# Performance work log

Hardware: AMD Instinct MI355X
Metric: run time of the kernel (lower is better)

The kernel has to match this reference:

```python
import jax, jax.numpy as jnp
import numpy as np

B, O, D = 64, 36, 512
G1, G2 = 512, 512  # interactor sizes
F1, F2 = 512, 512  # aggregator sizes
BN_EPS = 1e-5


def setup_inputs() -> dict:
    key = jax.random.key(0)
    ks = jax.random.split(key, 10)
    sc = 0.02
    return {
        "objs": jax.random.normal(ks[0], (B, O, D), jnp.float32),
        "W1": jax.random.normal(ks[1], (G1, 2 * D), jnp.float32) * sc,
        "b1": jax.random.normal(ks[2], (G1,), jnp.float32) * sc,
        "W2": jax.random.normal(ks[3], (G2, G1), jnp.float32) * sc,
        "b2": jax.random.normal(ks[4], (G2,), jnp.float32) * sc,
        "gamma": jnp.ones((G2,), jnp.float32),
        "beta": jnp.zeros((G2,), jnp.float32),
        "W3": jax.random.normal(ks[5], (F1, G2), jnp.float32) * sc,
        "b3": jax.random.normal(ks[6], (F1,), jnp.float32) * sc,
        "W4": jax.random.normal(ks[7], (F2, F1), jnp.float32) * sc,
        "b4": jax.random.normal(ks[8], (F2,), jnp.float32) * sc,
    }


def reference(objs, W1, b1, W2, b2, gamma, beta, W3, b3, W4, b4):
    b, o, d = objs.shape
    # make_pairs: x_full[b,k,m] = concat(v[b,m], v[b,k]) -> (b, o*o, 2d)
    v_i = jnp.broadcast_to(objs[:, None, :, :], (b, o, o, d))  # varies over m
    v_j = jnp.broadcast_to(objs[:, :, None, :], (b, o, o, d))  # varies over k
    pairs = jnp.concatenate([v_i, v_j], axis=-1).reshape(b, o * o, 2 * d)
    # interaction MLP g
    h = jax.nn.relu(jnp.einsum('bpc,gc->bpg', pairs, W1) + b1)
    x_pairs = jax.nn.relu(jnp.einsum('bpg,hg->bph', h, W2) + b2)
    # sum over pairs, BatchNorm1d (training mode: batch stats, biased var)
    s = x_pairs.sum(axis=1)  # (b, G2)
    mean = s.mean(axis=0)
    var = ((s - mean) ** 2).mean(axis=0)
    sn = (s - mean) / jnp.sqrt(var + BN_EPS) * gamma + beta
    # aggregation MLP f
    a = jax.nn.relu(sn @ W3.T + b3)
    agg = jax.nn.relu(a @ W4.T + b4)
    return agg, x_pairs
```

## Files before the change

### kernel.cpp

```cpp
#include <hip/hip_runtime.h>
#include <cstdint>
#include <cstddef>

#define B_  64
#define O_  36
#define D_  512
#define P_  (O_*O_)
#define BO_ (B_*O_)

typedef short s8v __attribute__((ext_vector_type(8)));
typedef float f4v __attribute__((ext_vector_type(4)));

__device__ __forceinline__ void bsplit(float x, short& hi, short& lo) {
    unsigned u = __float_as_uint(x);
    unsigned r = (u + 0x7FFFu + ((u >> 16) & 1u)) >> 16;
    hi = (short)r;
    float hf = __uint_as_float(r << 16);
    float d = x - hf;
    unsigned u2 = __float_as_uint(d);
    unsigned r2 = (u2 + 0x7FFFu + ((u2 >> 16) & 1u)) >> 16;
    lo = (short)r2;
}

__global__ __launch_bounds__(256) void w2split(
    const float* __restrict__ W2, short* __restrict__ hi, short* __restrict__ lo)
{
    const int i = (blockIdx.x * 256 + threadIdx.x) * 4;
    const float4 w = *(const float4*)&W2[i];
    short h0, l0, h1, l1, h2, l2, h3, l3;
    bsplit(w.x, h0, l0); bsplit(w.y, h1, l1);
    bsplit(w.z, h2, l2); bsplit(w.w, h3, l3);
    *(short4*)&hi[i] = make_short4(h0, h1, h2, h3);
    *(short4*)&lo[i] = make_short4(l0, l1, l2, l3);
}

__global__ __launch_bounds__(256) void w1split(
    const float* __restrict__ W1, short* __restrict__ hi, short* __restrict__ lo)
{
    const int i = (blockIdx.x * 256 + threadIdx.x) * 4;
    const int n = i >> 9, d = i & 511;
    const float4 w = *(const float4*)&W1[(size_t)(n & 511) * 1024 + ((n >> 9) << 9) + d];
    short h0, l0, h1, l1, h2, l2, h3, l3;
    bsplit(w.x, h0, l0); bsplit(w.y, h1, l1);
    bsplit(w.z, h2, l2); bsplit(w.w, h3, l3);
    *(short4*)&hi[i] = make_short4(h0, h1, h2, h3);
    *(short4*)&lo[i] = make_short4(l0, l1, l2, l3);
}

__global__ __launch_bounds__(256, 2) void uv_mfma(
    const float* __restrict__ objs,
    const short* __restrict__ W1h, const short* __restrict__ W1l,
    float* __restrict__ U, float* __restrict__ V)
{
    __shared__ short Ah[128 * 40];
    __shared__ short Al[128 * 40];
    __shared__ short Bh[128 * 40];
    __shared__ short Bl[128 * 40];

    const int tid  = threadIdx.x;
    const int lane = tid & 63;
    const int wid  = tid >> 6;
    const int wr   = wid >> 1, wc = wid & 1;
    const int rowbase = blockIdx.y * 128;
    const int colbase = blockIdx.x * 128;

    const int srow = tid >> 1;
    const int skq  = (tid & 1) * 8;
    const float* Xrow  = objs + (size_t)(rowbase + srow) * 512;
    const short* Whrow = W1h + (size_t)(colbase + srow) * 512;
    const short* Wlrow = W1l + (size_t)(colbase + srow) * 512;

    const int fr = lane & 15;
    const int sl = (lane >> 4) * 8;
    const int abase = (wr * 64 + fr) * 40 + sl;
    const int bbase = (wc * 64 + fr) * 40 + sl;

    f4v acc[4][4];
    const f4v zero = {0.f, 0.f, 0.f, 0.f};
    #pragma unroll
    for (int i = 0; i < 4; ++i)
        #pragma unroll
        for (int j = 0; j < 4; ++j) acc[i][j] = zero;

    for (int kt = 0; kt < 512; kt += 32) {
        __syncthreads();
        #pragma unroll
        for (int pass = 0; pass < 2; ++pass) {
            const int kq = skq + pass * 16;
            const float4 x0 = *(const float4*)&Xrow[kt + kq];
            const float4 x1 = *(const float4*)&Xrow[kt + kq + 4];
            float hx[8] = {x0.x, x0.y, x0.z, x0.w, x1.x, x1.y, x1.z, x1.w};
            s8v hi8, lo8;
            #pragma unroll
            for (int j = 0; j < 8; ++j) { short h, l; bsplit(hx[j], h, l); hi8[j] = h; lo8[j] = l; }
            *(s8v*)&Ah[srow * 40 + kq] = hi8;
            *(s8v*)&Al[srow * 40 + kq] = lo8;
            *(s8v*)&Bh[srow * 40 + kq] = *(const s8v*)&Whrow[kt + kq];
            *(s8v*)&Bl[srow * 40 + kq] = *(const s8v*)&Wlrow[kt + kq];
        }
        __syncthreads();

        s8v ah[4], al[4], bh[4], bl[4];
        #pragma unroll
        for (int f = 0; f < 4; ++f) {
            ah[f] = *(const s8v*)&Ah[abase + f * 640];
            al[f] = *(const s8v*)&Al[abase + f * 640];
            bh[f] = *(const s8v*)&Bh[bbase + f * 640];
            bl[f] = *(const s8v*)&Bl[bbase + f * 640];
        }
        #pragma unroll
        for (int fm = 0; fm < 4; ++fm)
            #pragma unroll
            for (int fn = 0; fn < 4; ++fn) {
                acc[fm][fn] = __builtin_amdgcn_mfma_f32_16x16x32_bf16(ah[fm], bh[fn], acc[fm][fn], 0, 0, 0);
                acc[fm][fn] = __builtin_amdgcn_mfma_f32_16x16x32_bf16(ah[fm], bl[fn], acc[fm][fn], 0, 0, 0);
                acc[fm][fn] = __builtin_amdgcn_mfma_f32_16x16x32_bf16(al[fm], bh[fn], acc[fm][fn], 0, 0, 0);
            }
    }

    float* dst = (colbase < 512) ? U : V;
    const int cb = colbase & 511;
    const int r4 = (lane >> 4) * 4;
    #pragma unroll
    for (int fm = 0; fm < 4; ++fm) {
        #pragma unroll
        for (int r = 0; r < 4; ++r) {
            const int row = rowbase + wr * 64 + fm * 16 + r4 + r;
            float* drow = &dst[(size_t)row * 512 + cb + wc * 64 + fr];
            #pragma unroll
            for (int fn = 0; fn < 4; ++fn) drow[fn * 16] = acc[fm][fn][r];
        }
    }
}

__global__ __launch_bounds__(256, 2) void pair_gemm(
    const float* __restrict__ U, const float* __restrict__ V,
    const float* __restrict__ b1,
    const short* __restrict__ W2h, const short* __restrict__ W2l,
    const float* __restrict__ b2,
    float* __restrict__ xout, float* __restrict__ s)
{
    __shared__ short Ah[128 * 40];
    __shared__ short Al[128 * 40];
    __shared__ short Bh[128 * 40];
    __shared__ short Bl[128 * 40];
    __shared__ float b1s[512];

    const int tid  = threadIdx.x;
    const int lane = tid & 63;
    const int wid  = tid >> 6;
    const int wr   = wid >> 1, wc = wid & 1;
    const int b       = blockIdx.z;
    const int pbase   = blockIdx.y * 128;
    const int colbase = blockIdx.x * 128;

    for (int g = tid; g < 512; g += 256) b1s[g] = b1[g];

    const int srow = tid >> 1;
    const int skq  = (tid & 1) * 8;
    const int p    = pbase + srow;
    const bool valid = (p < P_);
    int ki = 0, mi = 0;
    if (valid) { ki = p / O_; mi = p - ki * O_; }
    const float* Urow = U + (size_t)(b * O_ + mi) * 512;
    const float* Vrow = V + (size_t)(b * O_ + ki) * 512;
    const short* W2hrow = W2h + (size_t)(colbase + srow) * 512;
    const short* W2lrow = W2l + (size_t)(colbase + srow) * 512;

    const int fr = lane & 15;
    const int sl = (lane >> 4) * 8;
    const int abase = (wr * 64 + fr) * 40 + sl;
    const int bbase = (wc * 64 + fr) * 40 + sl;

    f4v acc[4][4];
    const f4v zero = {0.f, 0.f, 0.f, 0.f};
    #pragma unroll
    for (int i = 0; i < 4; ++i)
        #pragma unroll
        for (int j = 0; j < 4; ++j) acc[i][j] = zero;

    for (int kt = 0; kt < 512; kt += 32) {
        __syncthreads();
        #pragma unroll
        for (int pass = 0; pass < 2; ++pass) {
            const int kq = skq + pass * 16;
            s8v hi8, lo8;
            if (valid) {
                const float4 u0 = *(const float4*)&Urow[kt + kq];
                const float4 u1 = *(const float4*)&Urow[kt + kq + 4];
                const float4 v0 = *(const float4*)&Vrow[kt + kq];
                const float4 v1 = *(const float4*)&Vrow[kt + kq + 4];
                const float4 c0 = *(const float4*)&b1s[kt + kq];
                const float4 c1 = *(const float4*)&b1s[kt + kq + 4];
                float hx[8];
                hx[0] = fmaxf(u0.x + v0.x + c0.x, 0.f);
                hx[1] = fmaxf(u0.y + v0.y + c0.y, 0.f);
                hx[2] = fmaxf(u0.z + v0.z + c0.z, 0.f);
                hx[3] = fmaxf(u0.w + v0.w + c0.w, 0.f);
                hx[4] = fmaxf(u1.x + v1.x + c1.x, 0.f);
                hx[5] = fmaxf(u1.y + v1.y + c1.y, 0.f);
                hx[6] = fmaxf(u1.z + v1.z + c1.z, 0.f);
                hx[7] = fmaxf(u1.w + v1.w + c1.w, 0.f);
                #pragma unroll
                for (int j = 0; j < 8; ++j) { short h, l; bsplit(hx[j], h, l); hi8[j] = h; lo8[j] = l; }
            } else {
                #pragma unroll
                for (int j = 0; j < 8; ++j) { hi8[j] = 0; lo8[j] = 0; }
            }
            *(s8v*)&Ah[srow * 40 + kq] = hi8;
            *(s8v*)&Al[srow * 40 + kq] = lo8;
            *(s8v*)&Bh[srow * 40 + kq] = *(const s8v*)&W2hrow[kt + kq];
            *(s8v*)&Bl[srow * 40 + kq] = *(const s8v*)&W2lrow[kt + kq];
        }
        __syncthreads();

        s8v ah[4], al[4], bh[4], bl[4];
        #pragma unroll
        for (int f = 0; f < 4; ++f) {
            ah[f] = *(const s8v*)&Ah[abase + f * 640];
            al[f] = *(const s8v*)&Al[abase + f * 640];
            bh[f] = *(const s8v*)&Bh[bbase + f * 640];
            bl[f] = *(const s8v*)&Bl[bbase + f * 640];
        }
        #pragma unroll
        for (int fm = 0; fm < 4; ++fm)
            #pragma unroll
            for (int fn = 0; fn < 4; ++fn) {
                acc[fm][fn] = __builtin_amdgcn_mfma_f32_16x16x32_bf16(ah[fm], bh[fn], acc[fm][fn], 0, 0, 0);
                acc[fm][fn] = __builtin_amdgcn_mfma_f32_16x16x32_bf16(ah[fm], bl[fn], acc[fm][fn], 0, 0, 0);
                acc[fm][fn] = __builtin_amdgcn_mfma_f32_16x16x32_bf16(al[fm], bh[fn], acc[fm][fn], 0, 0, 0);
            }
    }

    float b2v[4];
    #pragma unroll
    for (int fn = 0; fn < 4; ++fn) b2v[fn] = b2[colbase + wc * 64 + fn * 16 + fr];
    const int r4 = (lane >> 4) * 4;
    float csum[4] = {0.f, 0.f, 0.f, 0.f};
    #pragma unroll
    for (int fm = 0; fm < 4; ++fm) {
        const int prow0 = pbase + wr * 64 + fm * 16 + r4;
        #pragma unroll
        for (int r = 0; r < 4; ++r) {
            const int pp = prow0 + r;
            if (pp < P_) {
                float* xrow = &xout[(size_t)(b * P_ + pp) * 512 + colbase + wc * 64 + fr];
                #pragma unroll
                for (int fn = 0; fn < 4; ++fn) {
                    float x = fmaxf(acc[fm][fn][r] + b2v[fn], 0.f);
                    xrow[fn * 16] = x;
                    csum[fn] += x;
                }
            }
        }
    }
    #pragma unroll
    for (int fn = 0; fn < 4; ++fn) {
        csum[fn] += __shfl_xor(csum[fn], 16);
        csum[fn] += __shfl_xor(csum[fn], 32);
    }
    if (lane < 16) {
        #pragma unroll
        for (int fn = 0; fn < 4; ++fn)
            atomicAdd(&s[b * 512 + colbase + wc * 64 + fn * 16 + lane], csum[fn]);
    }
}

__global__ __launch_bounds__(512) void bn_kernel(
    const float* __restrict__ s, const float* __restrict__ gamma,
    const float* __restrict__ beta, float* __restrict__ sn)
{
    const int g = threadIdx.x;
    float mean = 0.f;
    for (int b = 0; b < B_; ++b) mean += s[b * 512 + g];
    mean *= (1.f / B_);
    float var = 0.f;
    for (int b = 0; b < B_; ++b) { const float d = s[b * 512 + g] - mean; var = fmaf(d, d, var); }
    var *= (1.f / B_);
    const float inv = 1.f / sqrtf(var + 1e-5f);
    const float ga = gamma[g], be = beta[g];
    for (int b = 0; b < B_; ++b)
        sn[b * 512 + g] = (s[b * 512 + g] - mean) * inv * ga + be;
}

__global__ __launch_bounds__(256) void mlp512(
    const float* __restrict__ x, const float* __restrict__ W,
    const float* __restrict__ bias, float* __restrict__ out)
{
    __shared__ float xs[512];
    const int b = blockIdx.y;
    const int f = blockIdx.x * 256 + threadIdx.x;
    for (int g = threadIdx.x; g < 512; g += 256) xs[g] = x[b * 512 + g];
    __syncthreads();
    float sum = 0.f;
    #pragma unroll 8
    for (int k = 0; k < 512; k += 4) {
        const float4 w4 = *(const float4*)&W[(size_t)f * 512 + k];
        const float4 x4 = *(const float4*)&xs[k];
        sum = fmaf(w4.x, x4.x, sum); sum = fmaf(w4.y, x4.y, sum);
        sum = fmaf(w4.z, x4.z, sum); sum = fmaf(w4.w, x4.w, sum);
    }
    out[b * 512 + f] = fmaxf(sum + bias[f], 0.f);
}

extern "C" void kernel_launch(void* const* d_in, const int* in_sizes, int n_in,
                              void* d_out, int out_size, void* d_ws, size_t ws_size,
                              hipStream_t stream)
{
    const float* objs  = (const float*)d_in[0];
    const float* W1    = (const float*)d_in[1];
    const float* b1    = (const float*)d_in[2];
    const float* W2    = (const float*)d_in[3];
    const float* b2    = (const float*)d_in[4];
    const float* gamma = (const float*)d_in[5];
    const float* beta  = (const float*)d_in[6];
    const float* W3    = (const float*)d_in[7];
    const float* b3    = (const float*)d_in[8];
    const float* W4    = (const float*)d_in[9];
    const float* b4    = (const float*)d_in[10];

    float* out  = (float*)d_out;
    float* xout = out + B_ * 512;

    float* U  = (float*)d_ws;
    float* V  = U  + (size_t)BO_ * 512;
    float* s  = V  + (size_t)BO_ * 512;
    float* sn = s  + B_ * 512;
    float* a  = sn + B_ * 512;
    short* W2h = (short*)(a + B_ * 512);
    short* W2l = W2h + (size_t)512 * 512;
    short* W1h = W2l + (size_t)512 * 512;
    short* W1l = W1h + (size_t)1024 * 512;

    w2split<<<256, 256, 0, stream>>>(W2, W2h, W2l);
    w1split<<<512, 256, 0, stream>>>(W1, W1h, W1l);
    uv_mfma<<<dim3(8, 18), 256, 0, stream>>>(objs, W1h, W1l, U, V);
    hipMemsetAsync(s, 0, B_ * 512 * sizeof(float), stream);
    pair_gemm<<<dim3(4, 11, B_), 256, 0, stream>>>(U, V, b1, W2h, W2l, b2, xout, s);
    bn_kernel<<<1, 512, 0, stream>>>(s, gamma, beta, sn);
    mlp512<<<dim3(2, B_), 256, 0, stream>>>(sn, W3, b3, a);
    mlp512<<<dim3(2, B_), 256, 0, stream>>>(a, W4, b4, out);
}
```

Baseline: 434.5 us.

## Widen pair GEMM tiles to full 512 columns and fuse weight split kernels

The pair GEMM now runs 512-thread blocks that each cover all 512 output columns for a 128-pair tile. The hidden activation tile (U+V+b1, ReLU, bf16 split) is built once per block instead of once per column block, which removes the 4x recomputation and re-reading of U/V. The cost is a larger accumulator array (4x8 fragments per wave) and more LDS per block, which may hurt occupancy. The two weight-split kernels are merged into one launch, and the MFMA issue order in uv_mfma is regrouped.

```diff
diff --git a/kernel.cpp b/kernel.cpp
--- a/kernel.cpp
+++ b/kernel.cpp
@@ -22,29 +22,28 @@
     lo = (short)r2;
 }
 
-__global__ __launch_bounds__(256) void w2split(
-    const float* __restrict__ W2, short* __restrict__ hi, short* __restrict__ lo)
-{
-    const int i = (blockIdx.x * 256 + threadIdx.x) * 4;
-    const float4 w = *(const float4*)&W2[i];
+__global__ __launch_bounds__(256) void wsplit_all(
+    const float* __restrict__ W2, const float* __restrict__ W1,
+    short* __restrict__ W2h, short* __restrict__ W2l,
+    short* __restrict__ W1h, short* __restrict__ W1l)
+{
+    int i = (blockIdx.x * 256 + threadIdx.x) * 4;
+    float4 w;
+    short* hip_; short* lop_; int o;
+    if (i < 512 * 512) {
+        w = *(const float4*)&W2[i];
+        hip_ = W2h; lop_ = W2l; o = i;
+    } else {
+        o = i - 512 * 512;
+        const int n = o >> 9, d = o & 511;
+        w = *(const float4*)&W1[(size_t)(n & 511) * 1024 + ((n >> 9) << 9) + d];
+        hip_ = W1h; lop_ = W1l;
+    }
     short h0, l0, h1, l1, h2, l2, h3, l3;
     bsplit(w.x, h0, l0); bsplit(w.y, h1, l1);
     bsplit(w.z, h2, l2); bsplit(w.w, h3, l3);
-    *(short4*)&hi[i] = make_short4(h0, h1, h2, h3);
-    *(short4*)&lo[i] = make_short4(l0, l1, l2, l3);
-}
-
-__global__ __launch_bounds__(256) void w1split(
-    const float* __restrict__ W1, short* __restrict__ hi, short* __restrict__ lo)
-{
-    const int i = (blockIdx.x * 256 + threadIdx.x) * 4;
-    const int n = i >> 9, d = i & 511;
-    const float4 w = *(const float4*)&W1[(size_t)(n & 511) * 1024 + ((n >> 9) << 9) + d];
-    short h0, l0, h1, l1, h2, l2, h3, l3;
-    bsplit(w.x, h0, l0); bsplit(w.y, h1, l1);
-    bsplit(w.z, h2, l2); bsplit(w.w, h3, l3);
-    *(short4*)&hi[i] = make_short4(h0, h1, h2, h3);
-    *(short4*)&lo[i] = make_short4(l0, l1, l2, l3);
+    *(short4*)&hip_[o] = make_short4(h0, h1, h2, h3);
+    *(short4*)&lop_[o] = make_short4(l0, l1, l2, l3);
 }
 
 __global__ __launch_bounds__(256, 2) void uv_mfma(
@@ -111,11 +110,18 @@
         #pragma unroll
         for (int fm = 0; fm < 4; ++fm)
             #pragma unroll
-            for (int fn = 0; fn < 4; ++fn) {
+            for (int fn = 0; fn < 4; ++fn)
                 acc[fm][fn] = __builtin_amdgcn_mfma_f32_16x16x32_bf16(ah[fm], bh[fn], acc[fm][fn], 0, 0, 0);
+        #pragma unroll
+        for (int fm = 0; fm < 4; ++fm)
+            #pragma unroll
+            for (int fn = 0; fn < 4; ++fn)
                 acc[fm][fn] = __builtin_amdgcn_mfma_f32_16x16x32_bf16(ah[fm], bl[fn], acc[fm][fn], 0, 0, 0);
+        #pragma unroll
+        for (int fm = 0; fm < 4; ++fm)
+            #pragma unroll
+            for (int fn = 0; fn < 4; ++fn)
                 acc[fm][fn] = __builtin_amdgcn_mfma_f32_16x16x32_bf16(al[fm], bh[fn], acc[fm][fn], 0, 0, 0);
-            }
     }
 
     float* dst = (colbase < 512) ? U : V;
@@ -133,7 +139,7 @@
     }
 }
 
-__global__ __launch_bounds__(256, 2) void pair_gemm(
+__global__ __launch_bounds__(512, 2) void pair_gemm(
     const float* __restrict__ U, const float* __restrict__ V,
     const float* __restrict__ b1,
     const short* __restrict__ W2h, const short* __restrict__ W2l,
@@ -142,56 +148,55 @@
 {
     __shared__ short Ah[128 * 40];
     __shared__ short Al[128 * 40];
-    __shared__ short Bh[128 * 40];
-    __shared__ short Bl[128 * 40];
+    __shared__ short Bh[512 * 40];
+    __shared__ short Bl[512 * 40];
     __shared__ float b1s[512];
 
     const int tid  = threadIdx.x;
     const int lane = tid & 63;
     const int wid  = tid >> 6;
-    const int wr   = wid >> 1, wc = wid & 1;
-    const int b       = blockIdx.z;
-    const int pbase   = blockIdx.y * 128;
-    const int colbase = blockIdx.x * 128;
-
-    for (int g = tid; g < 512; g += 256) b1s[g] = b1[g];
-
-    const int srow = tid >> 1;
-    const int skq  = (tid & 1) * 8;
-    const int p    = pbase + srow;
+    const int wr   = wid >> 2;
+    const int wc   = wid & 3;
+    const int b     = blockIdx.y;
+    const int pbase = blockIdx.x * 128;
+
+    b1s[tid] = b1[tid];
+
+    const int arow = tid & 127;
+    const int akq  = (tid >> 7) << 3;
+    const int p    = pbase + arow;
     const bool valid = (p < P_);
     int ki = 0, mi = 0;
     if (valid) { ki = p / O_; mi = p - ki * O_; }
-    const float* Urow = U + (size_t)(b * O_ + mi) * 512;
-    const float* Vrow = V + (size_t)(b * O_ + ki) * 512;
-    const short* W2hrow = W2h + (size_t)(colbase + srow) * 512;
-    const short* W2lrow = W2l + (size_t)(colbase + srow) * 512;
+    const float* Urow = U + (size_t)(b * O_ + mi) * 512 + akq;
+    const float* Vrow = V + (size_t)(b * O_ + ki) * 512 + akq;
+
+    const short* Whrow = W2h + (size_t)tid * 512;
+    const short* Wlrow = W2l + (size_t)tid * 512;
 
     const int fr = lane & 15;
-    const int sl = (lane >> 4) * 8;
+    const int sl = (lane >> 4) << 3;
     const int abase = (wr * 64 + fr) * 40 + sl;
-    const int bbase = (wc * 64 + fr) * 40 + sl;
-
-    f4v acc[4][4];
+    const int bbase = (wc * 128 + fr) * 40 + sl;
+
+    f4v acc[4][8];
     const f4v zero = {0.f, 0.f, 0.f, 0.f};
     #pragma unroll
     for (int i = 0; i < 4; ++i)
         #pragma unroll
-        for (int j = 0; j < 4; ++j) acc[i][j] = zero;
+        for (int j = 0; j < 8; ++j) acc[i][j] = zero;
 
     for (int kt = 0; kt < 512; kt += 32) {
         __syncthreads();
-        #pragma unroll
-        for (int pass = 0; pass < 2; ++pass) {
-            const int kq = skq + pass * 16;
+        {
             s8v hi8, lo8;
             if (valid) {
-                const float4 u0 = *(const float4*)&Urow[kt + kq];
-                const float4 u1 = *(const float4*)&Urow[kt + kq + 4];
-                const float4 v0 = *(const float4*)&Vrow[kt + kq];
-                const float4 v1 = *(const float4*)&Vrow[kt + kq + 4];
-                const float4 c0 = *(const float4*)&b1s[kt + kq];
-                const float4 c1 = *(const float4*)&b1s[kt + kq + 4];
+                const float4 u0 = *(const float4*)&Urow[kt];
+                const float4 u1 = *(const float4*)&Urow[kt + 4];
+                const float4 v0 = *(const float4*)&Vrow[kt];
+                const float4 v1 = *(const float4*)&Vrow[kt + 4];
+                const float4 c0 = *(const float4*)&b1s[kt + akq];
+                const float4 c1 = *(const float4*)&b1s[kt + akq + 4];
                 float hx[8];
                 hx[0] = fmaxf(u0.x + v0.x + c0.x, 0.f);
                 hx[1] = fmaxf(u0.y + v0.y + c0.y, 0.f);
@@ -207,36 +212,43 @@
                 #pragma unroll
                 for (int j = 0; j < 8; ++j) { hi8[j] = 0; lo8[j] = 0; }
             }
-            *(s8v*)&Ah[srow * 40 + kq] = hi8;
-            *(s8v*)&Al[srow * 40 + kq] = lo8;
-            *(s8v*)&Bh[srow * 40 + kq] = *(const s8v*)&W2hrow[kt + kq];
-            *(s8v*)&Bl[srow * 40 + kq] = *(const s8v*)&W2lrow[kt + kq];
+            *(s8v*)&Ah[arow * 40 + akq] = hi8;
+            *(s8v*)&Al[arow * 40 + akq] = lo8;
+        }
+        #pragma unroll
+        for (int c = 0; c < 4; ++c) {
+            *(s8v*)&Bh[tid * 40 + c * 8] = *(const s8v*)&Whrow[kt + c * 8];
+            *(s8v*)&Bl[tid * 40 + c * 8] = *(const s8v*)&Wlrow[kt + c * 8];
         }
         __syncthreads();
 
-        s8v ah[4], al[4], bh[4], bl[4];
+        s8v ah[4], al[4];
         #pragma unroll
         for (int f = 0; f < 4; ++f) {
             ah[f] = *(const s8v*)&Ah[abase + f * 640];
             al[f] = *(const s8v*)&Al[abase + f * 640];
-            bh[f] = *(const s8v*)&Bh[bbase + f * 640];
-            bl[f] = *(const s8v*)&Bl[bbase + f * 640];
-        }
-        #pragma unroll
-        for (int fm = 0; fm < 4; ++fm)
-            #pragma unroll
-            for (int fn = 0; fn < 4; ++fn) {
-                acc[fm][fn] = __builtin_amdgcn_mfma_f32_16x16x32_bf16(ah[fm], bh[fn], acc[fm][fn], 0, 0, 0);
-                acc[fm][fn] = __builtin_amdgcn_mfma_f32_16x16x32_bf16(ah[fm], bl[fn], acc[fm][fn], 0, 0, 0);
-                acc[fm][fn] = __builtin_amdgcn_mfma_f32_16x16x32_bf16(al[fm], bh[fn], acc[fm][fn], 0, 0, 0);
-            }
-    }
-
-    float b2v[4];
-    #pragma unroll
-    for (int fn = 0; fn < 4; ++fn) b2v[fn] = b2[colbase + wc * 64 + fn * 16 + fr];
-    const int r4 = (lane >> 4) * 4;
-    float csum[4] = {0.f, 0.f, 0.f, 0.f};
+        }
+        #pragma unroll
+        for (int fn = 0; fn < 8; ++fn) {
+            const s8v bh = *(const s8v*)&Bh[bbase + fn * 640];
+            const s8v bl = *(const s8v*)&Bl[bbase + fn * 640];
+            #pragma unroll
+            for (int fm = 0; fm < 4; ++fm)
+                acc[fm][fn] = __builtin_amdgcn_mfma_f32_16x16x32_bf16(ah[fm], bh, acc[fm][fn], 0, 0, 0);
+            #pragma unroll
+            for (int fm = 0; fm < 4; ++fm)
+                acc[fm][fn] = __builtin_amdgcn_mfma_f32_16x16x32_bf16(ah[fm], bl, acc[fm][fn], 0, 0, 0);
+            #pragma unroll
+            for (int fm = 0; fm < 4; ++fm)
+                acc[fm][fn] = __builtin_amdgcn_mfma_f32_16x16x32_bf16(al[fm], bh, acc[fm][fn], 0, 0, 0);
+        }
+    }
+
+    float b2v[8];
+    #pragma unroll
+    for (int fn = 0; fn < 8; ++fn) b2v[fn] = b2[wc * 128 + fn * 16 + fr];
+    const int r4 = (lane >> 4) << 2;
+    float csum[8] = {0.f, 0.f, 0.f, 0.f, 0.f, 0.f, 0.f, 0.f};
     #pragma unroll
     for (int fm = 0; fm < 4; ++fm) {
         const int prow0 = pbase + wr * 64 + fm * 16 + r4;
@@ -244,9 +256,9 @@
         for (int r = 0; r < 4; ++r) {
             const int pp = prow0 + r;
             if (pp < P_) {
-                float* xrow = &xout[(size_t)(b * P_ + pp) * 512 + colbase + wc * 64 + fr];
+                float* xrow = &xout[(size_t)(b * P_ + pp) * 512 + wc * 128 + fr];
                 #pragma unroll
-                for (int fn = 0; fn < 4; ++fn) {
+                for (int fn = 0; fn < 8; ++fn) {
                     float x = fmaxf(acc[fm][fn][r] + b2v[fn], 0.f);
                     xrow[fn * 16] = x;
                     csum[fn] += x;
@@ -255,14 +267,14 @@
         }
     }
     #pragma unroll
-    for (int fn = 0; fn < 4; ++fn) {
+    for (int fn = 0; fn < 8; ++fn) {
         csum[fn] += __shfl_xor(csum[fn], 16);
         csum[fn] += __shfl_xor(csum[fn], 32);
     }
     if (lane < 16) {
         #pragma unroll
-        for (int fn = 0; fn < 4; ++fn)
-            atomicAdd(&s[b * 512 + colbase + wc * 64 + fn * 16 + lane], csum[fn]);
+        for (int fn = 0; fn < 8; ++fn)
+            atomicAdd(&s[b * 512 + wc * 128 + fn * 16 + lane], csum[fn]);
     }
 }
 
@@ -332,11 +344,10 @@
     short* W1h = W2l + (size_t)512 * 512;
     short* W1l = W1h + (size_t)1024 * 512;
 
-    w2split<<<256, 256, 0, stream>>>(W2, W2h, W2l);
-    w1split<<<512, 256, 0, stream>>>(W1, W1h, W1l);
+    wsplit_all<<<768, 256, 0, stream>>>(W2, W1, W2h, W2l, W1h, W1l);
     uv_mfma<<<dim3(8, 18), 256, 0, stream>>>(objs, W1h, W1l, U, V);
     hipMemsetAsync(s, 0, B_ * 512 * sizeof(float), stream);
-    pair_gemm<<<dim3(4, 11, B_), 256, 0, stream>>>(U, V, b1, W2h, W2l, b2, xout, s);
+    pair_gemm<<<dim3(11, 64), 512, 0, stream>>>(U, V, b1, W2h, W2l, b2, xout, s);
     bn_kernel<<<1, 512, 0, stream>>>(s, gamma, beta, sn);
     mlp512<<<dim3(2, B_), 256, 0, stream>>>(sn, W3, b3, a);
     mlp512<<<dim3(2, B_), 256, 0, stream>>>(a, W4, b4, out);
```

After: 469.4 us. 1.08x slower.
